# Performance work log

Measured on AMD Instinct MI355X. Metric: run time of the kernel, lower is better.

The kernel has to match this reference:

```python
import jax, jax.numpy as jnp
import numpy as np

DMODEL = 128
HEAD = 128
SEQ = 4096
BATCH = 16

def setup_inputs() -> dict:
    key = jax.random.key(0)
    kx, kq, kk, kv = jax.random.split(key, 4)
    x = jax.random.normal(kx, (BATCH, SEQ, DMODEL), dtype=jnp.float32)
    # nn.Linear(dmodel, head_size, bias=False): store as (dmodel, head_size) so q = x @ Wq
    s = 1.0 / np.sqrt(DMODEL)
    Wq = jax.random.uniform(kq, (DMODEL, HEAD), jnp.float32, -s, s)
    Wk = jax.random.uniform(kk, (DMODEL, HEAD), jnp.float32, -s, s)
    Wv = jax.random.uniform(kv, (DMODEL, HEAD), jnp.float32, -s, s)
    return {"x": x, "Wq": Wq, "Wk": Wk, "Wv": Wv}

def reference(x, Wq, Wk, Wv):
    B, L, _ = x.shape
    scale = HEAD ** (-0.5)
    q = jnp.einsum('bld,dh->blh', x, Wq)
    k = jnp.einsum('bld,dh->blh', x, Wk)
    v = jnp.einsum('bld,dh->blh', x, Wv)
    wei = jnp.einsum('bqh,bkh->bqk', q, k) * scale  # (B, L, L)
    causal = jnp.tril(jnp.ones((L, L), dtype=bool))
    wei = jnp.where(causal, wei, -jnp.inf)
    wei = jax.nn.softmax(wei, axis=-1)
    y = jnp.einsum('bqk,bkh->bqh', wei, v)
    return y
```

## Files before the change

kernel.cpp:

```cpp
#include <hip/hip_runtime.h>
#include <hip/hip_bf16.h>
#include <stdint.h>

#define SEQ   4096
#define DM    128
#define KVB   64

typedef __attribute__((ext_vector_type(8)))  short  bf16x8;
typedef __attribute__((ext_vector_type(16))) float  f32x16;

#define SCALE_LOG2E 0.12751743f

__device__ __forceinline__ f32x16 mfma_32x32x16(bf16x8 a, bf16x8 b, f32x16 c) {
  return __builtin_amdgcn_mfma_f32_32x32x16_bf16(a, b, c, 0, 0, 0);
}

__device__ __forceinline__ void gload16(const void* g, void* l) {
  __builtin_amdgcn_global_load_lds(
      (const __attribute__((address_space(1))) unsigned int*)g,
      (__attribute__((address_space(3))) unsigned int*)l, 16, 0, 0);
}

__device__ __forceinline__ unsigned pack2bf(float a, float b) {
  float2 t; t.x = a; t.y = b;
  __hip_bfloat162 h = __float22bfloat162_rn(t);
  union { __hip_bfloat162 h2; unsigned u; } cv;
  cv.h2 = h;
  return cv.u;
}

__device__ __forceinline__ float us2f(unsigned short u) {
  union { unsigned int i; float f; } c; c.i = ((unsigned)u) << 16; return c.f;
}

__device__ __forceinline__ float fast_exp2(float x) {
#if defined(__has_builtin)
#if __has_builtin(__builtin_amdgcn_exp2f)
  return __builtin_amdgcn_exp2f(x);
#else
  return exp2f(x);
#endif
#else
  return exp2f(x);
#endif
}

__global__ void prep_w(const float* __restrict__ Wq, const float* __restrict__ Wk,
                       const float* __restrict__ Wv, __hip_bfloat16* __restrict__ Wb) {
  int t = blockIdx.x * 256 + threadIdx.x;
  if (t >= 12 * 8 * 64) return;
  int ct  = t >> 9;
  int rem = t & 511;
  int s   = rem >> 6;
  int l   = rem & 63;
  const float* W = (ct < 4) ? Wq : (ct < 8) ? Wk : Wv;
  float c = (ct < 4) ? SCALE_LOG2E : 1.0f;
  int h  = (ct & 3) * 32 + (l & 31);
  int d0 = 16 * s + 8 * (l >> 5);
  union { __hip_bfloat16 h8[8]; bf16x8 v; } u;
#pragma unroll
  for (int i = 0; i < 8; ++i) u.h8[i] = __float2bfloat16(W[(d0 + i) * DM + h] * c);
  *(bf16x8*)&Wb[(size_t)t * 8] = u.v;
}

__global__ void __launch_bounds__(256, 2)
proj(const float* __restrict__ x, const __hip_bfloat16* __restrict__ Wb,
     __hip_bfloat16* __restrict__ qw, __hip_bfloat16* __restrict__ kw,
     __hip_bfloat16* __restrict__ vtw) {
  __shared__ __hip_bfloat16 slab[4][1024];
  const int wave = threadIdx.x >> 6, lane = threadIdx.x & 63;
  const int l31 = lane & 31, hi = lane >> 5;
  const int t0 = blockIdx.x * 128 + wave * 32;
  const int trow = t0 + l31;

  bf16x8 af[8];
#pragma unroll
  for (int s = 0; s < 8; ++s) {
    const float* px = x + (size_t)trow * DM + 16 * s + 8 * hi;
    float4 u0 = *(const float4*)px;
    float4 u1 = *(const float4*)(px + 4);
    union { bf16x8 v; unsigned u[4]; } fr;
    fr.u[0] = pack2bf(u0.x, u0.y);
    fr.u[1] = pack2bf(u0.z, u0.w);
    fr.u[2] = pack2bf(u1.x, u1.y);
    fr.u[3] = pack2bf(u1.z, u1.w);
    af[s] = fr.v;
  }

  for (int ct = 0; ct < 12; ++ct) {
    f32x16 acc;
#pragma unroll
    for (int j = 0; j < 16; ++j) acc[j] = 0.f;
#pragma unroll
    for (int s = 0; s < 8; ++s) {
      bf16x8 bfr = *(const bf16x8*)&Wb[(size_t)((ct * 8 + s) * 64 + lane) * 8];
      acc = mfma_32x32x16(af[s], bfr, acc);
    }
    __syncthreads();
#pragma unroll
    for (int j = 0; j < 16; ++j) {
      int r = (j & 3) + 8 * (j >> 2) + 4 * hi;
      slab[wave][r * 32 + l31] = __float2bfloat16(acc[j]);
    }
    __syncthreads();
    if (ct < 8) {
      __hip_bfloat16* dst = (ct < 4) ? qw : kw;
      int hb = (ct & 3) * 32;
#pragma unroll
      for (int p = 0; p < 2; ++p) {
        int eidx = p * 512 + lane * 8;
        int tr = eidx >> 5, c = eidx & 31;
        *(bf16x8*)&dst[(size_t)(t0 + tr) * DM + hb + c] =
            *(const bf16x8*)&slab[wave][eidx];
      }
    } else {
      int d  = lane >> 1;
      int th = (lane & 1) * 16;
      int dg = (ct & 3) * 32 + d;
      int bb = t0 >> 12;
      int tl = t0 & 4095;
      __hip_bfloat16* dst = vtw + ((size_t)bb * DM + dg) * SEQ + tl + th;
#pragma unroll
      for (int k = 0; k < 4; ++k) {
        union { unsigned short u4[4]; uint2 v; } pkv;
#pragma unroll
        for (int e = 0; e < 4; ++e) {
          union { __hip_bfloat16 hh; unsigned short us; } cv;
          cv.hh = slab[wave][(th + 4 * k + e) * 32 + d];
          pkv.u4[e] = cv.us;
        }
        *(uint2*)&dst[4 * k] = pkv.v;
      }
    }
  }
}

__device__ __forceinline__ void stage_k(const char* kb, int tile, char* kdst,
                                        int tid, int wave) {
  const char* ksrc = kb + (size_t)tile * (KVB * 256);
#pragma unroll
  for (int p = 0; p < 2; ++p) {
    int lin = p * 8192 + tid * 16;
    int row = lin >> 8, cb = lin & 255;
    int col = cb ^ ((row & 15) << 4);
    gload16(ksrc + row * 256 + col, kdst + p * 8192 + (wave << 10));
  }
}

__device__ __forceinline__ void stage_v(const char* vb, int tile, char* vdst,
                                        int tid, int wave) {
  const char* vsrc = vb + (size_t)tile * (KVB * 2);
#pragma unroll
  for (int p = 0; p < 2; ++p) {
    int lin = p * 8192 + tid * 16;
    int row = lin >> 8, cb = lin & 255;
    int col = cb ^ ((row & 15) << 4);
    size_t so = (size_t)(2 * row + (col >> 7)) * 8192 + (size_t)(col & 127);
    gload16(vsrc + so, vdst + p * 8192 + (wave << 10));
  }
}

__global__ void __launch_bounds__(512, 2)
attn(const __hip_bfloat16* __restrict__ qw, const __hip_bfloat16* __restrict__ kw,
     const __hip_bfloat16* __restrict__ vtw, float* __restrict__ out,
     float* __restrict__ lsumA, float* __restrict__ lsumB,
     __hip_bfloat16* __restrict__ partB) {
  __shared__ __align__(16) char lds[81920];
  const int bid = blockIdx.x;
  const int xcd = bid & 7;
  const int g   = bid >> 3;
  const int b   = xcd + 8 * (g & 1);
  const int j16 = g >> 1;
  const int i   = j16 & 7;
  const int isB = j16 >> 3;
  const int bigQ = 15 - i;
  const int m = b * 8 + i;

  const int wave = threadIdx.x >> 6, lane = threadIdx.x & 63;
  const int l31 = lane & 31, hi = lane >> 5;
  const int tid = threadIdx.x;

  const char* kb = (const char*)(kw + (size_t)b * SEQ * DM);
  const char* vb = (const char*)(vtw + (size_t)b * DM * SEQ);

  char* k_cur = lds;         char* k_nxt = lds + 16384; char* k_nn = lds + 32768;
  char* v_cur = lds + 49152; char* v_nxt = lds + 65536;

  auto visit = [&](int qt, int t0, int cnt, int mode) {
    const int q0 = qt << 8;
    const int qrow = q0 + wave * 32 + l31;
    const int qminw = q0 + wave * 32;
    const int qmaxw = qminw + 31;

    bf16x8 qf[8];
    {
      const __hip_bfloat16* qb = qw + ((size_t)b * SEQ + qrow) * DM;
#pragma unroll
      for (int s = 0; s < 8; ++s) qf[s] = *(const bf16x8*)&qb[16 * s + 8 * hi];
    }
    f32x16 yacc[4];
#pragma unroll
    for (int dt = 0; dt < 4; ++dt)
#pragma unroll
      for (int jj = 0; jj < 16; ++jj) yacc[dt][jj] = 0.f;
    f32x16 psum;
#pragma unroll
    for (int jj = 0; jj < 16; ++jj) psum[jj] = 0.f;

    stage_k(kb, t0, k_cur, tid, wave);
    stage_v(vb, t0, v_cur, tid, wave);
    stage_k(kb, (cnt > 1 ? t0 + 1 : t0), k_nxt, tid, wave);
    __builtin_amdgcn_sched_barrier(0);
    asm volatile("s_waitcnt vmcnt(2)" ::: "memory");
    __builtin_amdgcn_s_barrier();
    __builtin_amdgcn_sched_barrier(0);

    for (int u = 0; u < cnt; ++u) {
      const int t  = t0 + u;
      const int uv = (u + 1 < cnt) ? u + 1 : cnt - 1;
      const int uk = (u + 2 < cnt) ? u + 2 : cnt - 1;
      stage_v(vb, t0 + uv, v_nxt, tid, wave);
      stage_k(kb, t0 + uk, k_nn, tid, wave);

      const int kv0 = t * KVB;
      if (kv0 <= qmaxw) {
        f32x16 sa, sb;
#pragma unroll
        for (int jj = 0; jj < 16; ++jj) { sa[jj] = 0.f; sb[jj] = 0.f; }
        __builtin_amdgcn_s_setprio(1);
#pragma unroll
        for (int s = 0; s < 8; ++s) {
          int cbs = 32 * s + 16 * hi;
          int r0 = l31, r1 = l31 + 32;
          bf16x8 k0 = *(const bf16x8*)&k_cur[r0 * 256 + (cbs ^ ((r0 & 15) << 4))];
          bf16x8 k1 = *(const bf16x8*)&k_cur[r1 * 256 + (cbs ^ ((r1 & 15) << 4))];
          sa = mfma_32x32x16(k0, qf[s], sa);
          sb = mfma_32x32x16(k1, qf[s], sb);
        }
        __builtin_amdgcn_s_setprio(0);
        if (kv0 + 63 > qminw) {
#pragma unroll
          for (int jj = 0; jj < 16; ++jj) {
            int rr = (jj & 3) + 8 * (jj >> 2) + 4 * hi;
            sa[jj] = (kv0 + rr      > qrow) ? -1e30f : sa[jj];
            sb[jj] = (kv0 + 32 + rr > qrow) ? -1e30f : sb[jj];
          }
        }
#pragma unroll
        for (int jj = 0; jj < 16; ++jj) sa[jj] = fast_exp2(sa[jj]);
#pragma unroll
        for (int jj = 0; jj < 16; ++jj) sb[jj] = fast_exp2(sb[jj]);
#pragma unroll
        for (int jj = 0; jj < 16; ++jj) psum[jj] += sa[jj] + sb[jj];

#pragma unroll
        for (int a = 0; a < 2; ++a) {
          unsigned pk[8];
#pragma unroll
          for (int jj = 0; jj < 8; ++jj) {
            float lo  = a ? sb[2 * jj]     : sa[2 * jj];
            float hi2 = a ? sb[2 * jj + 1] : sa[2 * jj + 1];
            pk[jj] = pack2bf(lo, hi2);
          }
#pragma unroll
          for (int s2 = 0; s2 < 2; ++s2) {
            int base = 4 * s2;
            unsigned a0 = pk[base + 0], b0 = pk[base + 2];
            unsigned a1 = pk[base + 1], b1 = pk[base + 3];
            asm volatile("v_permlane32_swap_b32 %0, %1" : "+v"(a0), "+v"(b0));
            asm volatile("v_permlane32_swap_b32 %0, %1" : "+v"(a1), "+v"(b1));
            union { bf16x8 v; unsigned u[4]; } pf;
            pf.u[0] = a0;
            pf.u[1] = a1;
            pf.u[2] = b0;
            pf.u[3] = b1;
            __builtin_amdgcn_s_setprio(1);
#pragma unroll
            for (int dt = 0; dt < 4; ++dt) {
              int vrow = (l31 >> 1) + 16 * dt;
              int vcol = (l31 & 1) * 128 + 64 * a + 32 * s2 + 16 * hi;
              bf16x8 vf = *(const bf16x8*)&v_cur[vrow * 256 +
                                                 (vcol ^ ((vrow & 15) << 4))];
              yacc[dt] = mfma_32x32x16(vf, pf.v, yacc[dt]);
            }
            __builtin_amdgcn_s_setprio(0);
          }
        }
      }
      __builtin_amdgcn_sched_barrier(0);
      asm volatile("s_waitcnt vmcnt(2)" ::: "memory");
      __builtin_amdgcn_s_barrier();
      __builtin_amdgcn_sched_barrier(0);
      char* tmp = k_cur; k_cur = k_nxt; k_nxt = k_nn; k_nn = tmp;
      tmp = v_cur; v_cur = v_nxt; v_nxt = tmp;
    }
    __builtin_amdgcn_sched_barrier(0);
    asm volatile("s_waitcnt vmcnt(0)" ::: "memory");
    __builtin_amdgcn_s_barrier();
    __builtin_amdgcn_sched_barrier(0);

    float lsum = 0.f;
#pragma unroll
    for (int jj = 0; jj < 16; ++jj) lsum += psum[jj];
    lsum += __shfl_xor(lsum, 32);

    float* ob = out + ((size_t)b * SEQ + qrow) * DM;
    const int row = wave * 32 + l31;
    if (mode == 0) {
      float inv = 1.0f / lsum;
#pragma unroll
      for (int dt = 0; dt < 4; ++dt) {
#pragma unroll
        for (int g2 = 0; g2 < 4; ++g2) {
          float4 v;
          v.x = yacc[dt][4 * g2 + 0] * inv;
          v.y = yacc[dt][4 * g2 + 1] * inv;
          v.z = yacc[dt][4 * g2 + 2] * inv;
          v.w = yacc[dt][4 * g2 + 3] * inv;
          *(float4*)&ob[32 * dt + 8 * g2 + 4 * hi] = v;
        }
      }
    } else if (mode == 1) {
#pragma unroll
      for (int dt = 0; dt < 4; ++dt) {
#pragma unroll
        for (int g2 = 0; g2 < 4; ++g2) {
          float4 v;
          v.x = yacc[dt][4 * g2 + 0];
          v.y = yacc[dt][4 * g2 + 1];
          v.z = yacc[dt][4 * g2 + 2];
          v.w = yacc[dt][4 * g2 + 3];
          *(float4*)&ob[32 * dt + 8 * g2 + 4 * hi] = v;
        }
      }
      if (hi == 0) lsumA[m * 256 + row] = lsum;
    } else {
      __hip_bfloat16* pb = partB + ((size_t)m * 256 + row) * DM;
#pragma unroll
      for (int dt = 0; dt < 4; ++dt) {
#pragma unroll
        for (int g2 = 0; g2 < 4; ++g2) {
          uint2 pv;
          pv.x = pack2bf(yacc[dt][4 * g2 + 0], yacc[dt][4 * g2 + 1]);
          pv.y = pack2bf(yacc[dt][4 * g2 + 2], yacc[dt][4 * g2 + 3]);
          *(uint2*)&pb[32 * dt + 8 * g2 + 4 * hi] = pv;
        }
      }
      if (hi == 0) lsumB[m * 256 + row] = lsum;
    }
  };

  if (!isB) {
    visit(bigQ, 0, 34, 1);
  } else {
    visit(bigQ, 34, 30 - 4 * i, 2);
    visit(i, 0, 4 * i + 4, 0);
  }
}

__global__ void __launch_bounds__(256)
merge(float* __restrict__ out, const float* __restrict__ lsumA,
      const float* __restrict__ lsumB, const __hip_bfloat16* __restrict__ partB) {
  __shared__ float invls[256];
  const int m = blockIdx.x;
  const int b = m >> 3;
  const int Q = 15 - (m & 7);
  const int tid = threadIdx.x;
  invls[tid] = 1.0f / (lsumA[m * 256 + tid] + lsumB[m * 256 + tid]);
  __syncthreads();
  float4* o4 = (float4*)(out + ((size_t)b * SEQ + (size_t)Q * 256) * DM);
  const __hip_bfloat16* pb = partB + (size_t)m * 256 * DM;
#pragma unroll
  for (int k = 0; k < 32; ++k) {
    int e4 = tid + 256 * k;
    int row = e4 >> 5;
    float4 a = o4[e4];
    union { uint2 v; unsigned short s[4]; } pv;
    pv.v = *(const uint2*)&pb[e4 * 4];
    float inv = invls[row];
    float4 r;
    r.x = (a.x + us2f(pv.s[0])) * inv;
    r.y = (a.y + us2f(pv.s[1])) * inv;
    r.z = (a.z + us2f(pv.s[2])) * inv;
    r.w = (a.w + us2f(pv.s[3])) * inv;
    o4[e4] = r;
  }
}

extern "C" void kernel_launch(void* const* d_in, const int* in_sizes, int n_in,
                              void* d_out, int out_size, void* d_ws, size_t ws_size,
                              hipStream_t stream) {
  const float* x  = (const float*)d_in[0];
  const float* Wq = (const float*)d_in[1];
  const float* Wk = (const float*)d_in[2];
  const float* Wv = (const float*)d_in[3];
  float* out = (float*)d_out;

  char* ws = (char*)d_ws;
  __hip_bfloat16* qw    = (__hip_bfloat16*)(ws);
  __hip_bfloat16* kw    = (__hip_bfloat16*)(ws + (size_t)16 * 1024 * 1024);
  __hip_bfloat16* vtw   = (__hip_bfloat16*)(ws + (size_t)32 * 1024 * 1024);
  __hip_bfloat16* Wb    = (__hip_bfloat16*)(ws + (size_t)48 * 1024 * 1024);
  float*          lsumA = (float*)(ws + (size_t)48 * 1024 * 1024 + 128 * 1024);
  float*          lsumB = (float*)(ws + (size_t)48 * 1024 * 1024 + 256 * 1024);
  __hip_bfloat16* partB = (__hip_bfloat16*)(ws + (size_t)48 * 1024 * 1024 + 384 * 1024);

  prep_w<<<24, 256, 0, stream>>>(Wq, Wk, Wv, Wb);
  proj<<<512, 256, 0, stream>>>(x, Wb, qw, kw, vtw);
  attn<<<256, 512, 0, stream>>>(qw, kw, vtw, out, lsumA, lsumB, partB);
  merge<<<128, 256, 0, stream>>>(out, lsumA, lsumB, partB);
}
```

Measured before the change: 120.8 us.

## Software-pipeline QK^T of next KV tile with softmax and PV of current

Restructures the KV loop so the QK^T MFMAs for tile t+1 are issued in the same iteration as the exp2/pack/PV work for tile t. A prologue computes the first tile's scores, and K prefetch goes one tile deeper across the three K buffers. The aim is to hide softmax VALU and permlane latency behind matrix-core work. In exchange it holds two extra 16-float score accumulators per lane, which raises VGPR pressure, and it changes how many loads are outstanding when the vmcnt waits run.

New measurement: 122.5 us. No clear change (+1.3%).

```diff
diff --git a/kernel.cpp b/kernel.cpp
--- a/kernel.cpp
+++ b/kernel.cpp
@@ -44,6 +44,8 @@
   return exp2f(x);
 #endif
 }
+
+#define SBAR() __builtin_amdgcn_sched_barrier(0)
 
 __global__ void prep_w(const float* __restrict__ Wq, const float* __restrict__ Wk,
                        const float* __restrict__ Wv, __hip_bfloat16* __restrict__ Wb) {
@@ -183,14 +185,18 @@
   const char* kb = (const char*)(kw + (size_t)b * SEQ * DM);
   const char* vb = (const char*)(vtw + (size_t)b * DM * SEQ);
 
-  char* k_cur = lds;         char* k_nxt = lds + 16384; char* k_nn = lds + 32768;
-  char* v_cur = lds + 49152; char* v_nxt = lds + 65536;
-
   auto visit = [&](int qt, int t0, int cnt, int mode) {
     const int q0 = qt << 8;
     const int qrow = q0 + wave * 32 + l31;
     const int qminw = q0 + wave * 32;
     const int qmaxw = qminw + 31;
+    const int tlast = t0 + cnt - 1;
+
+    char* k0p = lds;
+    char* k1p = lds + 16384;
+    char* k2p = lds + 32768;
+    char* v0p = lds + 49152;
+    char* v1p = lds + 65536;
 
     bf16x8 qf[8];
     {
@@ -207,59 +213,83 @@
 #pragma unroll
     for (int jj = 0; jj < 16; ++jj) psum[jj] = 0.f;
 
-    stage_k(kb, t0, k_cur, tid, wave);
-    stage_v(vb, t0, v_cur, tid, wave);
-    stage_k(kb, (cnt > 1 ? t0 + 1 : t0), k_nxt, tid, wave);
-    __builtin_amdgcn_sched_barrier(0);
+    stage_k(kb, t0, k0p, tid, wave);
+    stage_v(vb, t0, v0p, tid, wave);
+    stage_k(kb, (1 < cnt ? t0 + 1 : tlast), k1p, tid, wave);
+    stage_k(kb, (2 < cnt ? t0 + 2 : tlast), k2p, tid, wave);
+    SBAR();
     asm volatile("s_waitcnt vmcnt(2)" ::: "memory");
     __builtin_amdgcn_s_barrier();
-    __builtin_amdgcn_sched_barrier(0);
+    SBAR();
+
+    f32x16 ca, cb2, na, nb;
+#pragma unroll
+    for (int jj = 0; jj < 16; ++jj) { ca[jj] = 0.f; cb2[jj] = 0.f; }
+    if (t0 * KVB <= qmaxw) {
+      __builtin_amdgcn_s_setprio(1);
+#pragma unroll
+      for (int s = 0; s < 8; ++s) {
+        int cbs = 32 * s + 16 * hi;
+        int r0 = l31, r1 = l31 + 32;
+        bf16x8 kk0 = *(const bf16x8*)&k0p[r0 * 256 + (cbs ^ ((r0 & 15) << 4))];
+        bf16x8 kk1 = *(const bf16x8*)&k0p[r1 * 256 + (cbs ^ ((r1 & 15) << 4))];
+        ca  = mfma_32x32x16(kk0, qf[s], ca);
+        cb2 = mfma_32x32x16(kk1, qf[s], cb2);
+      }
+      __builtin_amdgcn_s_setprio(0);
+    }
+    SBAR();
+    __builtin_amdgcn_s_barrier();
+    SBAR();
 
     for (int u = 0; u < cnt; ++u) {
       const int t  = t0 + u;
-      const int uv = (u + 1 < cnt) ? u + 1 : cnt - 1;
-      const int uk = (u + 2 < cnt) ? u + 2 : cnt - 1;
-      stage_v(vb, t0 + uv, v_nxt, tid, wave);
-      stage_k(kb, t0 + uk, k_nn, tid, wave);
-
-      const int kv0 = t * KVB;
-      if (kv0 <= qmaxw) {
-        f32x16 sa, sb;
-#pragma unroll
-        for (int jj = 0; jj < 16; ++jj) { sa[jj] = 0.f; sb[jj] = 0.f; }
+      const int tv = (u + 1 < cnt) ? t + 1 : tlast;
+      const int tk = (u + 3 < cnt) ? t + 3 : tlast;
+      stage_v(vb, tv, v1p, tid, wave);
+      stage_k(kb, tk, k0p, tid, wave);
+
+      const bool doqk = (u + 1 < cnt) && ((t + 1) * KVB <= qmaxw);
+#pragma unroll
+      for (int jj = 0; jj < 16; ++jj) { na[jj] = 0.f; nb[jj] = 0.f; }
+      if (doqk) {
         __builtin_amdgcn_s_setprio(1);
 #pragma unroll
         for (int s = 0; s < 8; ++s) {
           int cbs = 32 * s + 16 * hi;
           int r0 = l31, r1 = l31 + 32;
-          bf16x8 k0 = *(const bf16x8*)&k_cur[r0 * 256 + (cbs ^ ((r0 & 15) << 4))];
-          bf16x8 k1 = *(const bf16x8*)&k_cur[r1 * 256 + (cbs ^ ((r1 & 15) << 4))];
-          sa = mfma_32x32x16(k0, qf[s], sa);
-          sb = mfma_32x32x16(k1, qf[s], sb);
+          bf16x8 kk0 = *(const bf16x8*)&k1p[r0 * 256 + (cbs ^ ((r0 & 15) << 4))];
+          bf16x8 kk1 = *(const bf16x8*)&k1p[r1 * 256 + (cbs ^ ((r1 & 15) << 4))];
+          na = mfma_32x32x16(kk0, qf[s], na);
+          nb = mfma_32x32x16(kk1, qf[s], nb);
         }
         __builtin_amdgcn_s_setprio(0);
+      }
+
+      const int kv0 = t * KVB;
+      if (kv0 <= qmaxw) {
         if (kv0 + 63 > qminw) {
 #pragma unroll
           for (int jj = 0; jj < 16; ++jj) {
             int rr = (jj & 3) + 8 * (jj >> 2) + 4 * hi;
-            sa[jj] = (kv0 + rr      > qrow) ? -1e30f : sa[jj];
-            sb[jj] = (kv0 + 32 + rr > qrow) ? -1e30f : sb[jj];
+            ca[jj]  = (kv0 + rr      > qrow) ? -1e30f : ca[jj];
+            cb2[jj] = (kv0 + 32 + rr > qrow) ? -1e30f : cb2[jj];
           }
         }
 #pragma unroll
-        for (int jj = 0; jj < 16; ++jj) sa[jj] = fast_exp2(sa[jj]);
-#pragma unroll
-        for (int jj = 0; jj < 16; ++jj) sb[jj] = fast_exp2(sb[jj]);
-#pragma unroll
-        for (int jj = 0; jj < 16; ++jj) psum[jj] += sa[jj] + sb[jj];
+        for (int jj = 0; jj < 16; ++jj) ca[jj] = fast_exp2(ca[jj]);
+#pragma unroll
+        for (int jj = 0; jj < 16; ++jj) cb2[jj] = fast_exp2(cb2[jj]);
+#pragma unroll
+        for (int jj = 0; jj < 16; ++jj) psum[jj] += ca[jj] + cb2[jj];
 
 #pragma unroll
         for (int a = 0; a < 2; ++a) {
           unsigned pk[8];
 #pragma unroll
           for (int jj = 0; jj < 8; ++jj) {
-            float lo  = a ? sb[2 * jj]     : sa[2 * jj];
-            float hi2 = a ? sb[2 * jj + 1] : sa[2 * jj + 1];
+            float lo  = a ? cb2[2 * jj]     : ca[2 * jj];
+            float hi2 = a ? cb2[2 * jj + 1] : ca[2 * jj + 1];
             pk[jj] = pack2bf(lo, hi2);
           }
 #pragma unroll
@@ -279,25 +309,26 @@
             for (int dt = 0; dt < 4; ++dt) {
               int vrow = (l31 >> 1) + 16 * dt;
               int vcol = (l31 & 1) * 128 + 64 * a + 32 * s2 + 16 * hi;
-              bf16x8 vf = *(const bf16x8*)&v_cur[vrow * 256 +
-                                                 (vcol ^ ((vrow & 15) << 4))];
+              bf16x8 vf = *(const bf16x8*)&v0p[vrow * 256 +
+                                               (vcol ^ ((vrow & 15) << 4))];
               yacc[dt] = mfma_32x32x16(vf, pf.v, yacc[dt]);
             }
             __builtin_amdgcn_s_setprio(0);
           }
         }
       }
-      __builtin_amdgcn_sched_barrier(0);
+      SBAR();
       asm volatile("s_waitcnt vmcnt(2)" ::: "memory");
       __builtin_amdgcn_s_barrier();
-      __builtin_amdgcn_sched_barrier(0);
-      char* tmp = k_cur; k_cur = k_nxt; k_nxt = k_nn; k_nn = tmp;
-      tmp = v_cur; v_cur = v_nxt; v_nxt = tmp;
-    }
-    __builtin_amdgcn_sched_barrier(0);
+      SBAR();
+      char* tmpk = k0p; k0p = k1p; k1p = k2p; k2p = tmpk;
+      char* tmpv = v0p; v0p = v1p; v1p = tmpv;
+      ca = na; cb2 = nb;
+    }
+    SBAR();
     asm volatile("s_waitcnt vmcnt(0)" ::: "memory");
     __builtin_amdgcn_s_barrier();
-    __builtin_amdgcn_sched_barrier(0);
+    SBAR();
 
     float lsum = 0.f;
 #pragma unroll
```

## Split causal attention work into 512 equal 17-tile chunks with multi-slot merge

Applied to the files above, without the earlier changes.

Rebalances the causal attention work split. The old scheme used 256 blocks, each handling 34 KV tiles. The new one uses 512 blocks, each handling 17 KV tiles drawn from a paired high and low query tile, and splits long query rows across up to three partial slots that a wider merge kernel combines. Launch bounds are raised to request 4 blocks per CU, but each block still declares 80 KB of LDS, which likely caps real occupancy. The finer split aims for more parallelism and better load balance, at the cost of more partial-result traffic and merge work.

Measured after the change: 266.6 us. 2.21x slower.

```diff
diff --git a/kernel.cpp b/kernel.cpp
--- a/kernel.cpp
+++ b/kernel.cpp
@@ -44,6 +44,8 @@
   return exp2f(x);
 #endif
 }
+
+#define SBAR() __builtin_amdgcn_sched_barrier(0)
 
 __global__ void prep_w(const float* __restrict__ Wq, const float* __restrict__ Wk,
                        const float* __restrict__ Wv, __hip_bfloat16* __restrict__ Wb) {
@@ -160,21 +162,19 @@
   }
 }
 
-__global__ void __launch_bounds__(512, 2)
+__global__ void __launch_bounds__(512, 4)
 attn(const __hip_bfloat16* __restrict__ qw, const __hip_bfloat16* __restrict__ kw,
      const __hip_bfloat16* __restrict__ vtw, float* __restrict__ out,
-     float* __restrict__ lsumA, float* __restrict__ lsumB,
-     __hip_bfloat16* __restrict__ partB) {
+     float* __restrict__ lsumF, float* __restrict__ lsumS,
+     __hip_bfloat16* __restrict__ partS) {
   __shared__ __align__(16) char lds[81920];
   const int bid = blockIdx.x;
   const int xcd = bid & 7;
-  const int g   = bid >> 3;
-  const int b   = xcd + 8 * (g & 1);
-  const int j16 = g >> 1;
-  const int i   = j16 & 7;
-  const int isB = j16 >> 3;
-  const int bigQ = 15 - i;
-  const int m = b * 8 + i;
+  const int b   = xcd + 8 * ((bid >> 3) & 1);
+  const int s   = (bid >> 4) & 3;
+  const int g   = bid >> 6;
+  const int hiq = 15 - g, loq = g;
+  const int Lh  = 4 * hiq + 4;
 
   const int wave = threadIdx.x >> 6, lane = threadIdx.x & 63;
   const int l31 = lane & 31, hi = lane >> 5;
@@ -186,7 +186,7 @@
   char* k_cur = lds;         char* k_nxt = lds + 16384; char* k_nn = lds + 32768;
   char* v_cur = lds + 49152; char* v_nxt = lds + 65536;
 
-  auto visit = [&](int qt, int t0, int cnt, int mode) {
+  auto visit = [&](int qt, int t0, int cnt, int mode, int slot) {
     const int q0 = qt << 8;
     const int qrow = q0 + wave * 32 + l31;
     const int qminw = q0 + wave * 32;
@@ -196,7 +196,7 @@
     {
       const __hip_bfloat16* qb = qw + ((size_t)b * SEQ + qrow) * DM;
 #pragma unroll
-      for (int s = 0; s < 8; ++s) qf[s] = *(const bf16x8*)&qb[16 * s + 8 * hi];
+      for (int ss = 0; ss < 8; ++ss) qf[ss] = *(const bf16x8*)&qb[16 * ss + 8 * hi];
     }
     f32x16 yacc[4];
 #pragma unroll
@@ -210,10 +210,10 @@
     stage_k(kb, t0, k_cur, tid, wave);
     stage_v(vb, t0, v_cur, tid, wave);
     stage_k(kb, (cnt > 1 ? t0 + 1 : t0), k_nxt, tid, wave);
-    __builtin_amdgcn_sched_barrier(0);
+    SBAR();
     asm volatile("s_waitcnt vmcnt(2)" ::: "memory");
     __builtin_amdgcn_s_barrier();
-    __builtin_amdgcn_sched_barrier(0);
+    SBAR();
 
     for (int u = 0; u < cnt; ++u) {
       const int t  = t0 + u;
@@ -229,13 +229,13 @@
         for (int jj = 0; jj < 16; ++jj) { sa[jj] = 0.f; sb[jj] = 0.f; }
         __builtin_amdgcn_s_setprio(1);
 #pragma unroll
-        for (int s = 0; s < 8; ++s) {
-          int cbs = 32 * s + 16 * hi;
+        for (int ss = 0; ss < 8; ++ss) {
+          int cbs = 32 * ss + 16 * hi;
           int r0 = l31, r1 = l31 + 32;
           bf16x8 k0 = *(const bf16x8*)&k_cur[r0 * 256 + (cbs ^ ((r0 & 15) << 4))];
           bf16x8 k1 = *(const bf16x8*)&k_cur[r1 * 256 + (cbs ^ ((r1 & 15) << 4))];
-          sa = mfma_32x32x16(k0, qf[s], sa);
-          sb = mfma_32x32x16(k1, qf[s], sb);
+          sa = mfma_32x32x16(k0, qf[ss], sa);
+          sb = mfma_32x32x16(k1, qf[ss], sb);
         }
         __builtin_amdgcn_s_setprio(0);
         if (kv0 + 63 > qminw) {
@@ -287,17 +287,17 @@
           }
         }
       }
-      __builtin_amdgcn_sched_barrier(0);
+      SBAR();
       asm volatile("s_waitcnt vmcnt(2)" ::: "memory");
       __builtin_amdgcn_s_barrier();
-      __builtin_amdgcn_sched_barrier(0);
+      SBAR();
       char* tmp = k_cur; k_cur = k_nxt; k_nxt = k_nn; k_nn = tmp;
       tmp = v_cur; v_cur = v_nxt; v_nxt = tmp;
     }
-    __builtin_amdgcn_sched_barrier(0);
+    SBAR();
     asm volatile("s_waitcnt vmcnt(0)" ::: "memory");
     __builtin_amdgcn_s_barrier();
-    __builtin_amdgcn_sched_barrier(0);
+    SBAR();
 
     float lsum = 0.f;
 #pragma unroll
@@ -333,9 +333,9 @@
           *(float4*)&ob[32 * dt + 8 * g2 + 4 * hi] = v;
         }
       }
-      if (hi == 0) lsumA[m * 256 + row] = lsum;
+      if (hi == 0) lsumF[(b * 16 + qt) * 256 + row] = lsum;
     } else {
-      __hip_bfloat16* pb = partB + ((size_t)m * 256 + row) * DM;
+      __hip_bfloat16* pb = partS + ((size_t)slot * 256 + row) * DM;
 #pragma unroll
       for (int dt = 0; dt < 4; ++dt) {
 #pragma unroll
@@ -346,43 +346,64 @@
           *(uint2*)&pb[32 * dt + 8 * g2 + 4 * hi] = pv;
         }
       }
-      if (hi == 0) lsumB[m * 256 + row] = lsum;
+      if (hi == 0) lsumS[slot * 256 + row] = lsum;
     }
   };
 
-  if (!isB) {
-    visit(bigQ, 0, 34, 1);
-  } else {
-    visit(bigQ, 34, 30 - 4 * i, 2);
-    visit(i, 0, 4 * i + 4, 0);
+  auto slot_base = [](int q) {
+    return (q <= 7) ? (q - 4) : (q <= 11) ? (4 + (q - 8) * 2) : (12 + (q - 12) * 3);
+  };
+
+  const int g0 = 17 * s, g1 = g0 + 17;
+  if (g0 < Lh) {
+    int cnt = ((g1 < Lh) ? g1 : Lh) - g0;
+    int mode = (g0 == 0) ? 1 : 2;
+    int p = g0 / 17;
+    int slot = b * 24 + slot_base(hiq) + (p - 1);
+    visit(hiq, g0, cnt, mode, slot);
+  }
+  if (g1 > Lh) {
+    int st = (g0 > Lh) ? g0 : Lh;
+    int t0 = st - Lh;
+    int cnt = g1 - st;
+    int mode = (loq <= 3) ? 0 : ((t0 == 0) ? 1 : 2);
+    int slot = b * 24 + slot_base(loq);
+    visit(loq, t0, cnt, mode, slot);
   }
 }
 
 __global__ void __launch_bounds__(256)
-merge(float* __restrict__ out, const float* __restrict__ lsumA,
-      const float* __restrict__ lsumB, const __hip_bfloat16* __restrict__ partB) {
+merge(float* __restrict__ out, const float* __restrict__ lsumF,
+      const float* __restrict__ lsumS, const __hip_bfloat16* __restrict__ partS) {
   __shared__ float invls[256];
-  const int m = blockIdx.x;
-  const int b = m >> 3;
-  const int Q = 15 - (m & 7);
+  const int blk = blockIdx.x;
+  const int b = blk / 12;
+  const int q = (blk % 12) + 4;
+  const int nsl = (q <= 7) ? 1 : (q <= 11) ? 2 : 3;
+  const int s0 = b * 24 + ((q <= 7) ? (q - 4) : (q <= 11) ? (4 + (q - 8) * 2)
+                                               : (12 + (q - 12) * 3));
   const int tid = threadIdx.x;
-  invls[tid] = 1.0f / (lsumA[m * 256 + tid] + lsumB[m * 256 + tid]);
+  float ls = lsumF[(b * 16 + q) * 256 + tid];
+  for (int p = 0; p < nsl; ++p) ls += lsumS[(s0 + p) * 256 + tid];
+  invls[tid] = 1.0f / ls;
   __syncthreads();
-  float4* o4 = (float4*)(out + ((size_t)b * SEQ + (size_t)Q * 256) * DM);
-  const __hip_bfloat16* pb = partB + (size_t)m * 256 * DM;
+  float4* o4 = (float4*)(out + ((size_t)b * SEQ + (size_t)q * 256) * DM);
 #pragma unroll
   for (int k = 0; k < 32; ++k) {
     int e4 = tid + 256 * k;
     int row = e4 >> 5;
-    float4 a = o4[e4];
-    union { uint2 v; unsigned short s[4]; } pv;
-    pv.v = *(const uint2*)&pb[e4 * 4];
+    float4 r = o4[e4];
+    for (int p = 0; p < nsl; ++p) {
+      const __hip_bfloat16* pb = partS + (size_t)(s0 + p) * 256 * DM;
+      union { uint2 v; unsigned short sh[4]; } pv;
+      pv.v = *(const uint2*)&pb[e4 * 4];
+      r.x += us2f(pv.sh[0]);
+      r.y += us2f(pv.sh[1]);
+      r.z += us2f(pv.sh[2]);
+      r.w += us2f(pv.sh[3]);
+    }
     float inv = invls[row];
-    float4 r;
-    r.x = (a.x + us2f(pv.s[0])) * inv;
-    r.y = (a.y + us2f(pv.s[1])) * inv;
-    r.z = (a.z + us2f(pv.s[2])) * inv;
-    r.w = (a.w + us2f(pv.s[3])) * inv;
+    r.x *= inv; r.y *= inv; r.z *= inv; r.w *= inv;
     o4[e4] = r;
   }
 }
@@ -400,13 +421,14 @@
   __hip_bfloat16* qw    = (__hip_bfloat16*)(ws);
   __hip_bfloat16* kw    = (__hip_bfloat16*)(ws + (size_t)16 * 1024 * 1024);
   __hip_bfloat16* vtw   = (__hip_bfloat16*)(ws + (size_t)32 * 1024 * 1024);
-  __hip_bfloat16* Wb    = (__hip_bfloat16*)(ws + (size_t)48 * 1024 * 1024);
-  float*          lsumA = (float*)(ws + (size_t)48 * 1024 * 1024 + 128 * 1024);
-  float*          lsumB = (float*)(ws + (size_t)48 * 1024 * 1024 + 256 * 1024);
-  __hip_bfloat16* partB = (__hip_bfloat16*)(ws + (size_t)48 * 1024 * 1024 + 384 * 1024);
+  char* base48 = ws + (size_t)48 * 1024 * 1024;
+  __hip_bfloat16* Wb    = (__hip_bfloat16*)(base48);
+  float*          lsumF = (float*)(base48 + (size_t)1 * 1024 * 1024);
+  float*          lsumS = (float*)(base48 + (size_t)2 * 1024 * 1024);
+  __hip_bfloat16* partS = (__hip_bfloat16*)(base48 + (size_t)3 * 1024 * 1024);
 
   prep_w<<<24, 256, 0, stream>>>(Wq, Wk, Wv, Wb);
   proj<<<512, 256, 0, stream>>>(x, Wb, qw, kw, vtw);
-  attn<<<256, 512, 0, stream>>>(qw, kw, vtw, out, lsumA, lsumB, partB);
-  merge<<<128, 256, 0, stream>>>(out, lsumA, lsumB, partB);
-}
+  attn<<<512, 512, 0, stream>>>(qw, kw, vtw, out, lsumF, lsumS, partS);
+  merge<<<192, 256, 0, stream>>>(out, lsumF, lsumS, partS);
+}
```

## Double KV tile to 128 rows with two-stage double buffering in attention

Applied to the files above, without the earlier changes.

The attention kernel now stages 128-row K/V tiles instead of 64-row ones and processes each tile as two 64-row halves. The triple-buffered K pipeline with partial vmcnt waits becomes plain double buffering that waits for all loads before each barrier. The V LDS layout changes to row-major transposed rows, and the work split across blocks is rescaled to the new tile count. This halves the number of barriers per key range, but LDS use rises to 128KB, which drops the occupancy hint from two blocks per CU to one and removes the cross-iteration prefetch slack.

After: 120.2 us. No clear change (-0.6%).

```diff
diff --git a/kernel.cpp b/kernel.cpp
--- a/kernel.cpp
+++ b/kernel.cpp
@@ -4,7 +4,7 @@
 
 #define SEQ   4096
 #define DM    128
-#define KVB   64
+#define KVB   128
 
 typedef __attribute__((ext_vector_type(8)))  short  bf16x8;
 typedef __attribute__((ext_vector_type(16))) float  f32x16;
@@ -44,6 +44,8 @@
   return exp2f(x);
 #endif
 }
+
+#define SBAR() __builtin_amdgcn_sched_barrier(0)
 
 __global__ void prep_w(const float* __restrict__ Wq, const float* __restrict__ Wk,
                        const float* __restrict__ Wv, __hip_bfloat16* __restrict__ Wb) {
@@ -136,36 +138,35 @@
 }
 
 __device__ __forceinline__ void stage_k(const char* kb, int tile, char* kdst,
-                                        int tid, int wave) {
+                                        int tid) {
   const char* ksrc = kb + (size_t)tile * (KVB * 256);
 #pragma unroll
-  for (int p = 0; p < 2; ++p) {
+  for (int p = 0; p < 4; ++p) {
     int lin = p * 8192 + tid * 16;
     int row = lin >> 8, cb = lin & 255;
     int col = cb ^ ((row & 15) << 4);
-    gload16(ksrc + row * 256 + col, kdst + p * 8192 + (wave << 10));
+    gload16(ksrc + row * 256 + col, kdst + lin);
   }
 }
 
 __device__ __forceinline__ void stage_v(const char* vb, int tile, char* vdst,
-                                        int tid, int wave) {
+                                        int tid) {
   const char* vsrc = vb + (size_t)tile * (KVB * 2);
 #pragma unroll
-  for (int p = 0; p < 2; ++p) {
+  for (int p = 0; p < 4; ++p) {
     int lin = p * 8192 + tid * 16;
     int row = lin >> 8, cb = lin & 255;
     int col = cb ^ ((row & 15) << 4);
-    size_t so = (size_t)(2 * row + (col >> 7)) * 8192 + (size_t)(col & 127);
-    gload16(vsrc + so, vdst + p * 8192 + (wave << 10));
-  }
-}
-
-__global__ void __launch_bounds__(512, 2)
+    gload16(vsrc + (size_t)row * 8192 + col, vdst + lin);
+  }
+}
+
+__global__ void __launch_bounds__(512)
 attn(const __hip_bfloat16* __restrict__ qw, const __hip_bfloat16* __restrict__ kw,
      const __hip_bfloat16* __restrict__ vtw, float* __restrict__ out,
      float* __restrict__ lsumA, float* __restrict__ lsumB,
      __hip_bfloat16* __restrict__ partB) {
-  __shared__ __align__(16) char lds[81920];
+  __shared__ __align__(16) char lds[131072];
   const int bid = blockIdx.x;
   const int xcd = bid & 7;
   const int g   = bid >> 3;
@@ -183,8 +184,8 @@
   const char* kb = (const char*)(kw + (size_t)b * SEQ * DM);
   const char* vb = (const char*)(vtw + (size_t)b * DM * SEQ);
 
-  char* k_cur = lds;         char* k_nxt = lds + 16384; char* k_nn = lds + 32768;
-  char* v_cur = lds + 49152; char* v_nxt = lds + 65536;
+  char* k_cur = lds;         char* k_nxt = lds + 32768;
+  char* v_cur = lds + 65536; char* v_nxt = lds + 98304;
 
   auto visit = [&](int qt, int t0, int cnt, int mode) {
     const int q0 = qt << 8;
@@ -196,7 +197,7 @@
     {
       const __hip_bfloat16* qb = qw + ((size_t)b * SEQ + qrow) * DM;
 #pragma unroll
-      for (int s = 0; s < 8; ++s) qf[s] = *(const bf16x8*)&qb[16 * s + 8 * hi];
+      for (int ss = 0; ss < 8; ++ss) qf[ss] = *(const bf16x8*)&qb[16 * ss + 8 * hi];
     }
     f32x16 yacc[4];
 #pragma unroll
@@ -207,35 +208,35 @@
 #pragma unroll
     for (int jj = 0; jj < 16; ++jj) psum[jj] = 0.f;
 
-    stage_k(kb, t0, k_cur, tid, wave);
-    stage_v(vb, t0, v_cur, tid, wave);
-    stage_k(kb, (cnt > 1 ? t0 + 1 : t0), k_nxt, tid, wave);
-    __builtin_amdgcn_sched_barrier(0);
-    asm volatile("s_waitcnt vmcnt(2)" ::: "memory");
+    stage_k(kb, t0, k_cur, tid);
+    stage_v(vb, t0, v_cur, tid);
+    SBAR();
+    asm volatile("s_waitcnt vmcnt(0)" ::: "memory");
     __builtin_amdgcn_s_barrier();
-    __builtin_amdgcn_sched_barrier(0);
+    SBAR();
 
     for (int u = 0; u < cnt; ++u) {
       const int t  = t0 + u;
-      const int uv = (u + 1 < cnt) ? u + 1 : cnt - 1;
-      const int uk = (u + 2 < cnt) ? u + 2 : cnt - 1;
-      stage_v(vb, t0 + uv, v_nxt, tid, wave);
-      stage_k(kb, t0 + uk, k_nn, tid, wave);
-
-      const int kv0 = t * KVB;
-      if (kv0 <= qmaxw) {
+      const int un = (u + 1 < cnt) ? u + 1 : u;
+      stage_k(kb, t0 + un, k_nxt, tid);
+      stage_v(vb, t0 + un, v_nxt, tid);
+
+#pragma unroll
+      for (int h = 0; h < 2; ++h) {
+        const int kv0 = t * KVB + 64 * h;
+        if (kv0 > qmaxw) continue;
         f32x16 sa, sb;
 #pragma unroll
         for (int jj = 0; jj < 16; ++jj) { sa[jj] = 0.f; sb[jj] = 0.f; }
         __builtin_amdgcn_s_setprio(1);
 #pragma unroll
-        for (int s = 0; s < 8; ++s) {
-          int cbs = 32 * s + 16 * hi;
-          int r0 = l31, r1 = l31 + 32;
+        for (int ss = 0; ss < 8; ++ss) {
+          int cbs = 32 * ss + 16 * hi;
+          int r0 = 64 * h + l31, r1 = 64 * h + l31 + 32;
           bf16x8 k0 = *(const bf16x8*)&k_cur[r0 * 256 + (cbs ^ ((r0 & 15) << 4))];
           bf16x8 k1 = *(const bf16x8*)&k_cur[r1 * 256 + (cbs ^ ((r1 & 15) << 4))];
-          sa = mfma_32x32x16(k0, qf[s], sa);
-          sb = mfma_32x32x16(k1, qf[s], sb);
+          sa = mfma_32x32x16(k0, qf[ss], sa);
+          sb = mfma_32x32x16(k1, qf[ss], sb);
         }
         __builtin_amdgcn_s_setprio(0);
         if (kv0 + 63 > qminw) {
@@ -277,8 +278,8 @@
             __builtin_amdgcn_s_setprio(1);
 #pragma unroll
             for (int dt = 0; dt < 4; ++dt) {
-              int vrow = (l31 >> 1) + 16 * dt;
-              int vcol = (l31 & 1) * 128 + 64 * a + 32 * s2 + 16 * hi;
+              int vrow = 32 * dt + l31;
+              int vcol = 128 * h + 64 * a + 32 * s2 + 16 * hi;
               bf16x8 vf = *(const bf16x8*)&v_cur[vrow * 256 +
                                                  (vcol ^ ((vrow & 15) << 4))];
               yacc[dt] = mfma_32x32x16(vf, pf.v, yacc[dt]);
@@ -287,17 +288,13 @@
           }
         }
       }
-      __builtin_amdgcn_sched_barrier(0);
-      asm volatile("s_waitcnt vmcnt(2)" ::: "memory");
+      SBAR();
+      asm volatile("s_waitcnt vmcnt(0)" ::: "memory");
       __builtin_amdgcn_s_barrier();
-      __builtin_amdgcn_sched_barrier(0);
-      char* tmp = k_cur; k_cur = k_nxt; k_nxt = k_nn; k_nn = tmp;
+      SBAR();
+      char* tmp = k_cur; k_cur = k_nxt; k_nxt = tmp;
       tmp = v_cur; v_cur = v_nxt; v_nxt = tmp;
     }
-    __builtin_amdgcn_sched_barrier(0);
-    asm volatile("s_waitcnt vmcnt(0)" ::: "memory");
-    __builtin_amdgcn_s_barrier();
-    __builtin_amdgcn_sched_barrier(0);
 
     float lsum = 0.f;
 #pragma unroll
@@ -351,10 +348,10 @@
   };
 
   if (!isB) {
-    visit(bigQ, 0, 34, 1);
+    visit(bigQ, 0, 17, 1);
   } else {
-    visit(bigQ, 34, 30 - 4 * i, 2);
-    visit(i, 0, 4 * i + 4, 0);
+    visit(bigQ, 17, 15 - 2 * i, 2);
+    visit(i, 0, 2 * i + 2, 0);
   }
 }
 
@@ -400,10 +397,11 @@
   __hip_bfloat16* qw    = (__hip_bfloat16*)(ws);
   __hip_bfloat16* kw    = (__hip_bfloat16*)(ws + (size_t)16 * 1024 * 1024);
   __hip_bfloat16* vtw   = (__hip_bfloat16*)(ws + (size_t)32 * 1024 * 1024);
-  __hip_bfloat16* Wb    = (__hip_bfloat16*)(ws + (size_t)48 * 1024 * 1024);
-  float*          lsumA = (float*)(ws + (size_t)48 * 1024 * 1024 + 128 * 1024);
-  float*          lsumB = (float*)(ws + (size_t)48 * 1024 * 1024 + 256 * 1024);
-  __hip_bfloat16* partB = (__hip_bfloat16*)(ws + (size_t)48 * 1024 * 1024 + 384 * 1024);
+  char* base48 = ws + (size_t)48 * 1024 * 1024;
+  __hip_bfloat16* Wb    = (__hip_bfloat16*)(base48);
+  float*          lsumA = (float*)(base48 + (size_t)1 * 1024 * 1024);
+  float*          lsumB = (float*)(base48 + (size_t)2 * 1024 * 1024);
+  __hip_bfloat16* partB = (__hip_bfloat16*)(base48 + (size_t)3 * 1024 * 1024);
 
   prep_w<<<24, 256, 0, stream>>>(Wq, Wk, Wv, Wb);
   proj<<<512, 256, 0, stream>>>(x, Wb, qw, kw, vtw);
```
